# Kernel tuning notes

Measured on AMD Instinct MI355X. Metric: run time of the kernel, lower is better.

Reference implementation:

```python
import jax, jax.numpy as jnp
import numpy as np

H = 16            # num heads
D = 64            # head dim
HID = 1024        # hidden size
ALPHA = 1.0       # < 2 -> power-law kernel
BANDWIDTH = 1.0
A = 0.5           # doubly-stochastic exponent
RADIUS = 1.0      # sphere radius
EPS = 1e-7


def setup_inputs() -> dict:
    key = jax.random.key(0)
    ks = jax.random.split(key, 5)
    x = jax.random.normal(ks[0], (2, 2048, HID), dtype=jnp.float32)
    s = 1.0 / np.sqrt(HID)
    qkv_w = jax.random.normal(ks[1], (3 * HID, HID), dtype=jnp.float32) * s
    qkv_b = jnp.zeros((3 * HID,), dtype=jnp.float32)
    out_w = jax.random.normal(ks[2], (HID, HID), dtype=jnp.float32) * s
    out_b = jnp.zeros((HID,), dtype=jnp.float32)
    return {"x": x, "qkv_w": qkv_w, "qkv_b": qkv_b, "out_w": out_w, "out_b": out_b}


def _l2norm(t):
    # torch F.normalize(p=2, dim=-1): divide by max(||t||, 1e-12)
    n = jnp.sqrt(jnp.sum(t * t, axis=-1, keepdims=True))
    return t / jnp.maximum(n, 1e-12)


def reference(x, qkv_w, qkv_b, out_w, out_b):
    B, S, _ = x.shape
    qkv = x @ qkv_w.T + qkv_b                       # [B,S,3*HID]
    q, k, v = jnp.split(qkv, 3, axis=-1)
    # [B,H,S,D]
    q = _l2norm(q.reshape(B, S, H, D).transpose(0, 2, 1, 3))
    k = _l2norm(k.reshape(B, S, H, D).transpose(0, 2, 1, 3))
    v = v.reshape(B, S, H, D).transpose(0, 2, 1, 3)
    # geodesic distance on the sphere
    cos = jnp.clip(jnp.einsum('bhsd,bhtd->bhst', q, k), -1.0 + EPS, 1.0 - EPS)
    g_dist = jnp.arccos(cos) * RADIUS               # [B,H,S,S]
    # alpha < 2: power-law kernel
    attn_score = (1.0 + g_dist / jnp.sqrt(BANDWIDTH)) ** (-(D + ALPHA))
    # doubly-stochastic-style rescale: diag(row^-a) @ K @ diag(col^-a)
    row = attn_score.sum(-1) ** (-A)                # [B,H,S]
    col = attn_score.sum(-2) ** (-A)                # [B,H,S]
    k_tilde = row[..., :, None] * attn_score * col[..., None, :]
    # F.normalize(p=1, dim=3): divide by max(sum |.|, 1e-12); entries >= 0
    probs = k_tilde / jnp.maximum(k_tilde.sum(-1, keepdims=True), 1e-12)
    out = jnp.einsum('bhst,bhtd->bhsd', probs, v)   # [B,H,S,D]
    out = out.transpose(0, 2, 1, 3).reshape(B, S, HID)
    return out @ out_w.T + out_b
```

## Files before the change

### kernel.cpp

```cpp
#include <hip/hip_runtime.h>
#include <math.h>

#define NH   16
#define HD   64
#define HIDN 1024
#define NB   2
#define SEQ  2048
#define ROWS (NB*SEQ)
#define BH   (NB*NH)

typedef __attribute__((ext_vector_type(8))) short bf16x8;
typedef __attribute__((ext_vector_type(8))) _Float16 f16x8;
typedef __attribute__((ext_vector_type(4))) float f32x4;
typedef __attribute__((ext_vector_type(2))) float f32x2;
typedef _Float16 f16;

typedef const __attribute__((address_space(1))) void GV;
typedef __attribute__((address_space(3))) void LV;
__device__ __forceinline__ void glds16(const void* g, void* l) {
    __builtin_amdgcn_global_load_lds((GV*)g, (LV*)l, 16, 0, 0);
}

__device__ __forceinline__ unsigned short f2bf(float f) {
    unsigned u = __float_as_uint(f);
    u += 0x7FFF + ((u >> 16) & 1);
    return (unsigned short)(u >> 16);
}
__device__ __forceinline__ bf16x8 ldfrag(const unsigned short* p) {
    return *(const bf16x8*)p;
}
__device__ __forceinline__ f16x8 ldfragh(const f16* p) {
    return *(const f16x8*)p;
}
__device__ __forceinline__ f32x4 mfma16(bf16x8 a, bf16x8 b, f32x4 c) {
    return __builtin_amdgcn_mfma_f32_16x16x32_bf16(a, b, c, 0, 0, 0);
}
__device__ __forceinline__ f32x4 mfma16h(f16x8 a, f16x8 b, f32x4 c) {
    return __builtin_amdgcn_mfma_f32_16x16x32_f16(a, b, c, 0, 0, 0);
}

__device__ __forceinline__ f32x2 log2_1pacos_pair(float c0, float c1) {
    f32x2 u = { fmaxf(1.0f - c0, 0.0f), fmaxf(1.0f - c1, 0.0f) };
    f32x2 s = { __builtin_amdgcn_sqrtf(u.x), __builtin_amdgcn_sqrtf(u.y) };
    f32x2 p = u * 2.68532e-3f + 7.89259e-3f;
    p = u * p + 2.6516504e-2f;
    p = u * p + 1.1785113e-1f;
    p = u * p + 1.4142136f;
    f32x2 t = s * p + 1.0f;
    return (f32x2){ __builtin_amdgcn_logf(t.x), __builtin_amdgcn_logf(t.y) };
}
__device__ __forceinline__ unsigned packbf(f32x2 w) {
    return (__float_as_uint(w.x) >> 16) | (__float_as_uint(w.y) & 0xffff0000u);
}

__global__ __launch_bounds__(256)
void conv_f16(const float* __restrict__ src, f16* __restrict__ dst) {
    int i = (blockIdx.x * 256 + threadIdx.x) * 8;
    float4 a = *(const float4*)(src + i);
    float4 b = *(const float4*)(src + i + 4);
    f16x8 o = { (f16)a.x, (f16)a.y, (f16)a.z, (f16)a.w,
                (f16)b.x, (f16)b.y, (f16)b.z, (f16)b.w };
    *(f16x8*)(dst + i) = o;
}

__global__ __launch_bounds__(256)
void gemm_nt_f16(const f16* __restrict__ A, const f16* __restrict__ B,
                 const float* __restrict__ bias, float* __restrict__ C,
                 int M, int N, int K)
{
    __shared__ f16 As[128 * 32];
    __shared__ f16 Bs[128 * 32];
    const int tid = threadIdx.x;
    const int lane = tid & 63, w = tid >> 6;
    const int ln = lane & 15, lq = lane >> 4;
    const int wm = (w >> 1) * 64, wn = (w & 1) * 64;
    const int m0 = blockIdx.x * 128, n0 = blockIdx.y * 128;

    const int grow = lane >> 2;
    const int gcol = (lane & 3) * 8;
    const f16* Ab = A + (size_t)(m0 + w * 32 + grow) * K + gcol;
    const f16* Bb = B + (size_t)(n0 + w * 32 + grow) * K + gcol;
    f16* Asw = As + (w * 32) * 32;
    f16* Bsw = Bs + (w * 32) * 32;

    f32x4 acc[4][4];
    #pragma unroll
    for (int i = 0; i < 4; ++i)
        #pragma unroll
        for (int j = 0; j < 4; ++j) acc[i][j] = (f32x4){0.f, 0.f, 0.f, 0.f};

    for (int kc = 0; kc < K; kc += 32) {
        __syncthreads();
        #pragma unroll
        for (int i = 0; i < 2; ++i) {
            glds16(Ab + (size_t)(i * 16) * K + kc, Asw + (i * 16) * 32);
            glds16(Bb + (size_t)(i * 16) * K + kc, Bsw + (i * 16) * 32);
        }
        __syncthreads();
        f16x8 af[4], bf[4];
        #pragma unroll
        for (int i = 0; i < 4; ++i)
            af[i] = *(const f16x8*)&As[(wm + i * 16 + ln) * 32 + lq * 8];
        #pragma unroll
        for (int j = 0; j < 4; ++j)
            bf[j] = *(const f16x8*)&Bs[(wn + j * 16 + ln) * 32 + lq * 8];
        #pragma unroll
        for (int i = 0; i < 4; ++i)
            #pragma unroll
            for (int j = 0; j < 4; ++j)
                acc[i][j] = mfma16h(af[i], bf[j], acc[i][j]);
    }

    #pragma unroll
    for (int i = 0; i < 4; ++i) {
        #pragma unroll
        for (int j = 0; j < 4; ++j) {
            int colIdx = n0 + wn + j * 16 + ln;
            float bs = bias[colIdx];
            #pragma unroll
            for (int r = 0; r < 4; ++r) {
                int row = m0 + wm + i * 16 + lq * 4 + r;
                C[(size_t)row * N + colIdx] = acc[i][j][r] + bs;
            }
        }
    }
}

__global__ __launch_bounds__(256)
void normalize_qk_f16(const float* __restrict__ qkv,
                      f16* __restrict__ qf, f16* __restrict__ kf)
{
    int w    = blockIdx.x * 4 + (threadIdx.x >> 6);
    int lane = threadIdx.x & 63;
    int n = w >> 4, h = w & 15;
    int b = n >> 11, s = n & 2047;
    const float* base = qkv + (size_t)n * 3 * HIDN + h * HD;
    float q = base[lane], k = base[HIDN + lane];
    float qs = q * q, ks = k * k;
    #pragma unroll
    for (int o = 32; o; o >>= 1) { qs += __shfl_xor(qs, o); ks += __shfl_xor(ks, o); }
    q *= 1.0f / fmaxf(sqrtf(qs), 1e-12f);
    k *= 1.0f / fmaxf(sqrtf(ks), 1e-12f);
    size_t idx = ((size_t)((b * NH + h) * SEQ + s)) * HD + lane;
    qf[idx] = (f16)q;
    kf[idx] = (f16)k;
}

__global__ __launch_bounds__(256)
void v_transpose(const float* __restrict__ qkv, unsigned short* __restrict__ vth)
{
    __shared__ float Ls[64][65];
    int bh = blockIdx.y, s0 = blockIdx.x * 64;
    int b = bh >> 4, h = bh & 15;
    int tid = threadIdx.x;
    #pragma unroll
    for (int i = 0; i < 4; ++i) {
        int idx = tid + i * 256;
        int row = idx >> 4, c4 = (idx & 15) * 4;
        float4 v = *(const float4*)&qkv[((size_t)(b * SEQ + s0 + row)) * 3 * HIDN
                                        + 2 * HIDN + h * HD + c4];
        Ls[row][c4+0] = v.x; Ls[row][c4+1] = v.y; Ls[row][c4+2] = v.z; Ls[row][c4+3] = v.w;
    }
    __syncthreads();
    int d = tid >> 2, sb = (tid & 3) * 16;
    unsigned short hi[16];
    #pragma unroll
    for (int j = 0; j < 16; ++j) hi[j] = f2bf(Ls[sb + j][d]);
    size_t o = ((size_t)bh * HD + d) * SEQ + s0 + sb;
    *(uint4*)&vth[o]     = *(uint4*)&hi[0];
    *(uint4*)&vth[o + 8] = *(uint4*)&hi[8];
}

#define KSTR 72
#define VSTR 40
#define WSTR 40

__global__ __launch_bounds__(256)
void col_sum_f16(const f16* __restrict__ qf, const f16* __restrict__ kf,
                 float* __restrict__ colp)
{
    __shared__ __align__(16) f16 Qs[64 * KSTR];
    int bh = blockIdx.y;
    int tid = threadIdx.x, w = tid >> 6, lane = tid & 63, ln = lane & 15, lq = lane >> 4;
    int m0 = blockIdx.x * 64 + w * 16;
    const int sb0 = blockIdx.z * (SEQ / 128);
    const f16* qb = qf + (size_t)bh * SEQ * HD;
    const int sr = tid >> 3;
    const int sc = (tid & 7) * 8;

    size_t rowK = ((size_t)bh * SEQ + m0 + ln) * HD;
    f16x8 kf0 = ldfragh(kf + rowK + lq * 8), kf1 = ldfragh(kf + rowK + 32 + lq * 8);

    uint4 qa = *(const uint4*)(qb + (size_t)(sb0 * 64 + sr) * HD + sc);
    uint4 qc = *(const uint4*)(qb + (size_t)(sb0 * 64 + sr + 32) * HD + sc);

    f32x2 cacc01 = {0.f, 0.f}, cacc23 = {0.f, 0.f};
    #pragma unroll 1
    for (int st = sb0; st < sb0 + SEQ / 128; ++st) {
        __syncthreads();
        *(uint4*)&Qs[sr * KSTR + sc] = qa;
        *(uint4*)&Qs[(sr + 32) * KSTR + sc] = qc;
        int sn = (st + 1 < sb0 + SEQ / 128) ? (st + 1) * 64 : sb0 * 64;
        qa = *(const uint4*)(qb + (size_t)(sn + sr) * HD + sc);
        qc = *(const uint4*)(qb + (size_t)(sn + sr + 32) * HD + sc);
        __syncthreads();
        #pragma unroll
        for (int nt = 0; nt < 4; ++nt) {
            const f16* qp = &Qs[(nt * 16 + ln) * KSTR + lq * 8];
            f32x4 sacc = {0.f, 0.f, 0.f, 0.f};
            sacc = mfma16h(kf0, *(const f16x8*)qp, sacc);
            sacc = mfma16h(kf1, *(const f16x8*)(qp + 32), sacc);
            f32x2 l01 = log2_1pacos_pair(sacc[0], sacc[1]) * -65.0f;
            f32x2 l23 = log2_1pacos_pair(sacc[2], sacc[3]) * -65.0f;
            cacc01 += (f32x2){ __builtin_amdgcn_exp2f(l01.x),
                               __builtin_amdgcn_exp2f(l01.y) };
            cacc23 += (f32x2){ __builtin_amdgcn_exp2f(l23.x),
                               __builtin_amdgcn_exp2f(l23.y) };
        }
    }
    float cacc[4] = {cacc01.x, cacc01.y, cacc23.x, cacc23.y};
    #pragma unroll
    for (int r = 0; r < 4; ++r) {
        float v = cacc[r];
        v += __shfl_xor(v, 1); v += __shfl_xor(v, 2);
        v += __shfl_xor(v, 4); v += __shfl_xor(v, 8);
        if (ln == 0)
            colp[(size_t)blockIdx.z * BH * SEQ + (size_t)bh * SEQ + m0 + lq * 4 + r] = v;
    }
}

__global__ __launch_bounds__(256)
void col_finalize(const float* __restrict__ colp, float* __restrict__ col)
{
    int i = (blockIdx.x * 256 + threadIdx.x) * 4;
    float4 a = *(const float4*)&colp[i];
    float4 b = *(const float4*)&colp[(size_t)BH * SEQ + i];
    float4 o;
    o.x = -0.5f * __builtin_amdgcn_logf(a.x + b.x);
    o.y = -0.5f * __builtin_amdgcn_logf(a.y + b.y);
    o.z = -0.5f * __builtin_amdgcn_logf(a.z + b.z);
    o.w = -0.5f * __builtin_amdgcn_logf(a.w + b.w);
    *(float4*)&col[i] = o;
}

__global__ __launch_bounds__(256)
void attn_f16(const f16* __restrict__ qf, const f16* __restrict__ kf,
              const unsigned short* __restrict__ vth,
              const float* __restrict__ col,
              float* __restrict__ numb, float* __restrict__ denb)
{
    __shared__ __align__(16) f16 Ks[32 * KSTR];
    __shared__ __align__(16) unsigned short Vs[64 * VSTR];
    __shared__ __align__(16) unsigned short Ws[4][16 * WSTR];
    __shared__ __align__(16) float lcls[32];
    int bh = blockIdx.y;
    int b = bh >> 4, h = bh & 15;
    int tid = threadIdx.x, w = tid >> 6, lane = tid & 63, ln = lane & 15, lq = lane >> 4;
    int m0 = blockIdx.x * 64 + w * 16;
    const int th = blockIdx.z;
    const int tb = th * (SEQ / 2);
    unsigned short* ws = Ws[w];

    const f16* kb = kf + (size_t)bh * SEQ * HD;
    const unsigned short* vb = vth + (size_t)bh * HD * SEQ;
    const float* cb = col + (size_t)bh * SEQ;

    const int krow = tid >> 3;
    const int kcol = (tid & 7) * 8;
    const int vrow = tid >> 2;
    const int vcol = (tid & 3) * 8;

    size_t rowQ = ((size_t)bh * SEQ + m0 + ln) * HD;
    f16x8 qf0 = ldfragh(qf + rowQ + lq * 8), qf1 = ldfragh(qf + rowQ + 32 + lq * 8);

    bf16x8 ones;
    #pragma unroll
    for (int i = 0; i < 8; ++i) ones[i] = (short)0x3F80;

    f32x4 num[4];
    #pragma unroll
    for (int nt = 0; nt < 4; ++nt) num[nt] = (f32x4){0.f, 0.f, 0.f, 0.f};
    f32x4 den = {0.f, 0.f, 0.f, 0.f};

    uint4 ka = *(const uint4*)(kb + (size_t)(tb + krow) * HD + kcol);
    uint4 va = *(const uint4*)(vb + (size_t)vrow * SEQ + tb + vcol);
    float clv = (tid < 32) ? cb[tb + tid] : 0.f;

    #pragma unroll 1
    for (int tt = 0; tt < SEQ / 64; ++tt) {
        __syncthreads();
        *(uint4*)&Ks[krow * KSTR + kcol] = ka;
        *(uint4*)&Vs[vrow * VSTR + vcol] = va;
        if (tid < 32) lcls[tid] = clv;
        int tn = (tt + 1 < SEQ / 64) ? tb + (tt + 1) * 32 : tb;
        ka = *(const uint4*)(kb + (size_t)(tn + krow) * HD + kcol);
        va = *(const uint4*)(vb + (size_t)vrow * SEQ + tn + vcol);
        clv = (tid < 32) ? cb[tn + tid] : 0.f;
        __syncthreads();

        #pragma unroll
        for (int nt = 0; nt < 2; ++nt) {
            const f16* kp = &Ks[(nt * 16 + ln) * KSTR + lq * 8];
            f32x4 sacc = {0.f, 0.f, 0.f, 0.f};
            sacc = mfma16h(*(const f16x8*)kp, qf0, sacc);
            sacc = mfma16h(*(const f16x8*)(kp + 32), qf1, sacc);
            float4 cl = *(const float4*)&lcls[nt * 16 + lq * 4];
            f32x2 a01 = log2_1pacos_pair(sacc[0], sacc[1]) * -65.0f
                        + (f32x2){cl.x, cl.y};
            f32x2 a23 = log2_1pacos_pair(sacc[2], sacc[3]) * -65.0f
                        + (f32x2){cl.z, cl.w};
            f32x2 w01 = { __builtin_amdgcn_exp2f(a01.x),
                          __builtin_amdgcn_exp2f(a01.y) };
            f32x2 w23 = { __builtin_amdgcn_exp2f(a23.x),
                          __builtin_amdgcn_exp2f(a23.y) };
            uint2 pw;
            pw.x = packbf(w01);
            pw.y = packbf(w23);
            *(uint2*)(ws + ln * WSTR + nt * 16 + lq * 4) = pw;
        }
        bf16x8 wa0 = ldfrag(ws + ln * WSTR + lq * 8);
        den = mfma16(wa0, ones, den);
        #pragma unroll
        for (int nt = 0; nt < 4; ++nt) {
            const unsigned short* vp = &Vs[(nt * 16 + ln) * VSTR + lq * 8];
            num[nt] = mfma16(wa0, *(const bf16x8*)vp, num[nt]);
        }
    }

    const size_t noff = (size_t)th * ROWS * HIDN;
    #pragma unroll
    for (int r = 0; r < 4; ++r) {
        int s = m0 + lq * 4 + r;
        #pragma unroll
        for (int nt = 0; nt < 4; ++nt)
            numb[noff + ((size_t)(b * SEQ + s)) * HIDN + h * HD + nt * 16 + ln] =
                num[nt][r];
        if (ln == 0)
            denb[(size_t)th * BH * SEQ + (size_t)bh * SEQ + s] = den[r];
    }
}

__global__ __launch_bounds__(256)
void finalize_ctx(const float* __restrict__ numb, const float* __restrict__ denb,
                  f16* __restrict__ ctx)
{
    size_t i = ((size_t)blockIdx.x * 256 + threadIdx.x) * 8;
    int row = (int)(i >> 10);
    int cidx = (int)(i & (HIDN - 1));
    int b = row >> 11, s = row & 2047;
    int h = cidx >> 6;
    size_t di = (size_t)(b * NH + h) * SEQ + s;
    float d = denb[di] + denb[(size_t)BH * SEQ + di];
    float inv = 1.0f / fmaxf(d, 1e-12f);
    const float* n1 = numb + (size_t)ROWS * HIDN;
    float4 a0 = *(const float4*)&numb[i];
    float4 a1 = *(const float4*)&numb[i + 4];
    float4 b0 = *(const float4*)&n1[i];
    float4 b1 = *(const float4*)&n1[i + 4];
    f16x8 o = { (f16)((a0.x + b0.x) * inv), (f16)((a0.y + b0.y) * inv),
                (f16)((a0.z + b0.z) * inv), (f16)((a0.w + b0.w) * inv),
                (f16)((a1.x + b1.x) * inv), (f16)((a1.y + b1.y) * inv),
                (f16)((a1.z + b1.z) * inv), (f16)((a1.w + b1.w) * inv) };
    *(f16x8*)(ctx + i) = o;
}

extern "C" void kernel_launch(void* const* d_in, const int* in_sizes, int n_in,
                              void* d_out, int out_size, void* d_ws, size_t ws_size,
                              hipStream_t stream) {
    const float* x      = (const float*)d_in[0];
    const float* qkv_w  = (const float*)d_in[1];
    const float* qkv_b  = (const float*)d_in[2];
    const float* out_w  = (const float*)d_in[3];
    const float* out_b  = (const float*)d_in[4];
    float* out = (float*)d_out;

    const size_t NTT = (size_t)BH * SEQ * HD;
    float* qkv = (float*)d_ws;
    float* colp = qkv;
    float* denb = qkv + 2 * (size_t)BH * SEQ;
    float* numb = qkv + 4 * (size_t)BH * SEQ;
    float* col = qkv + (size_t)ROWS * 3 * HIDN;
    f16* xh    = (f16*)(col + (size_t)BH * SEQ);
    f16* wqh   = xh + (size_t)ROWS * HIDN;
    f16* woh   = wqh + (size_t)3 * HIDN * HIDN;
    f16* ctxh  = woh + (size_t)HIDN * HIDN;
    f16* qfp   = ctxh + (size_t)ROWS * HIDN;
    f16* kfp   = qfp + NTT;
    unsigned short* vth = (unsigned short*)(kfp + NTT);

    conv_f16<<<ROWS*HIDN/2048, 256, 0, stream>>>(x, xh);
    conv_f16<<<3*HIDN*HIDN/2048, 256, 0, stream>>>(qkv_w, wqh);
    conv_f16<<<HIDN*HIDN/2048, 256, 0, stream>>>(out_w, woh);

    gemm_nt_f16<<<dim3(ROWS/128, 3*HIDN/128), 256, 0, stream>>>(
        xh, wqh, qkv_b, qkv, ROWS, 3*HIDN, HIDN);
    normalize_qk_f16<<<ROWS*NH/4, 256, 0, stream>>>(qkv, qfp, kfp);
    v_transpose<<<dim3(SEQ/64, BH), 256, 0, stream>>>(qkv, vth);
    col_sum_f16<<<dim3(SEQ/64, BH, 2), 256, 0, stream>>>(qfp, kfp, colp);
    col_finalize<<<BH*SEQ/1024, 256, 0, stream>>>(colp, col);
    attn_f16<<<dim3(SEQ/64, BH, 2), 256, 0, stream>>>(qfp, kfp, vth, col,
                                                      numb, denb);
    finalize_ctx<<<ROWS*HIDN/2048, 256, 0, stream>>>(numb, denb, ctxh);
    gemm_nt_f16<<<dim3(ROWS/128, HIDN/128), 256, 0, stream>>>(
        ctxh, woh, out_b, out, ROWS, HIDN, HIDN);
}
```

Before: 331.4 us.

## Load K/Q/V MFMA fragments directly from global memory, dropping LDS staging and barriers

In the column-sum and attention kernels, the cooperative LDS staging of Q, K, V and column scales, along with the two __syncthreads per tile, is removed. Each wave now reads its MFMA fragments straight from global memory, relying on L1/L2 for reuse across the four waves of a block. The attention tile also grows from 32 to 64 keys per iteration, issuing two bf16 MFMAs per V subtile. This cuts barrier and LDS traffic but leaves more latency exposed on global loads, since the explicit register prefetch of the next tile is gone.

```diff
diff --git a/kernel.cpp b/kernel.cpp
--- a/kernel.cpp
+++ b/kernel.cpp
@@ -171,45 +171,32 @@
     *(uint4*)&vth[o + 8] = *(uint4*)&hi[8];
 }
 
-#define KSTR 72
-#define VSTR 40
-#define WSTR 40
+#define WSTR 72
 
 __global__ __launch_bounds__(256)
 void col_sum_f16(const f16* __restrict__ qf, const f16* __restrict__ kf,
                  float* __restrict__ colp)
 {
-    __shared__ __align__(16) f16 Qs[64 * KSTR];
     int bh = blockIdx.y;
     int tid = threadIdx.x, w = tid >> 6, lane = tid & 63, ln = lane & 15, lq = lane >> 4;
     int m0 = blockIdx.x * 64 + w * 16;
-    const int sb0 = blockIdx.z * (SEQ / 128);
+    const int sb0 = blockIdx.z * (SEQ / 2);
     const f16* qb = qf + (size_t)bh * SEQ * HD;
-    const int sr = tid >> 3;
-    const int sc = (tid & 7) * 8;
 
     size_t rowK = ((size_t)bh * SEQ + m0 + ln) * HD;
     f16x8 kf0 = ldfragh(kf + rowK + lq * 8), kf1 = ldfragh(kf + rowK + 32 + lq * 8);
 
-    uint4 qa = *(const uint4*)(qb + (size_t)(sb0 * 64 + sr) * HD + sc);
-    uint4 qc = *(const uint4*)(qb + (size_t)(sb0 * 64 + sr + 32) * HD + sc);
-
     f32x2 cacc01 = {0.f, 0.f}, cacc23 = {0.f, 0.f};
     #pragma unroll 1
-    for (int st = sb0; st < sb0 + SEQ / 128; ++st) {
-        __syncthreads();
-        *(uint4*)&Qs[sr * KSTR + sc] = qa;
-        *(uint4*)&Qs[(sr + 32) * KSTR + sc] = qc;
-        int sn = (st + 1 < sb0 + SEQ / 128) ? (st + 1) * 64 : sb0 * 64;
-        qa = *(const uint4*)(qb + (size_t)(sn + sr) * HD + sc);
-        qc = *(const uint4*)(qb + (size_t)(sn + sr + 32) * HD + sc);
-        __syncthreads();
+    for (int st = 0; st < SEQ / 128; ++st) {
+        int s0 = sb0 + st * 64;
         #pragma unroll
         for (int nt = 0; nt < 4; ++nt) {
-            const f16* qp = &Qs[(nt * 16 + ln) * KSTR + lq * 8];
+            const f16* qp = qb + (size_t)(s0 + nt * 16 + ln) * HD + lq * 8;
+            f16x8 qa = ldfragh(qp), qc = ldfragh(qp + 32);
             f32x4 sacc = {0.f, 0.f, 0.f, 0.f};
-            sacc = mfma16h(kf0, *(const f16x8*)qp, sacc);
-            sacc = mfma16h(kf1, *(const f16x8*)(qp + 32), sacc);
+            sacc = mfma16h(kf0, qa, sacc);
+            sacc = mfma16h(kf1, qc, sacc);
             f32x2 l01 = log2_1pacos_pair(sacc[0], sacc[1]) * -65.0f;
             f32x2 l23 = log2_1pacos_pair(sacc[2], sacc[3]) * -65.0f;
             cacc01 += (f32x2){ __builtin_amdgcn_exp2f(l01.x),
@@ -249,10 +236,7 @@
               const float* __restrict__ col,
               float* __restrict__ numb, float* __restrict__ denb)
 {
-    __shared__ __align__(16) f16 Ks[32 * KSTR];
-    __shared__ __align__(16) unsigned short Vs[64 * VSTR];
     __shared__ __align__(16) unsigned short Ws[4][16 * WSTR];
-    __shared__ __align__(16) float lcls[32];
     int bh = blockIdx.y;
     int b = bh >> 4, h = bh & 15;
     int tid = threadIdx.x, w = tid >> 6, lane = tid & 63, ln = lane & 15, lq = lane >> 4;
@@ -265,11 +249,6 @@
     const unsigned short* vb = vth + (size_t)bh * HD * SEQ;
     const float* cb = col + (size_t)bh * SEQ;
 
-    const int krow = tid >> 3;
-    const int kcol = (tid & 7) * 8;
-    const int vrow = tid >> 2;
-    const int vcol = (tid & 3) * 8;
-
     size_t rowQ = ((size_t)bh * SEQ + m0 + ln) * HD;
     f16x8 qf0 = ldfragh(qf + rowQ + lq * 8), qf1 = ldfragh(qf + rowQ + 32 + lq * 8);
 
@@ -282,29 +261,17 @@
     for (int nt = 0; nt < 4; ++nt) num[nt] = (f32x4){0.f, 0.f, 0.f, 0.f};
     f32x4 den = {0.f, 0.f, 0.f, 0.f};
 
-    uint4 ka = *(const uint4*)(kb + (size_t)(tb + krow) * HD + kcol);
-    uint4 va = *(const uint4*)(vb + (size_t)vrow * SEQ + tb + vcol);
-    float clv = (tid < 32) ? cb[tb + tid] : 0.f;
-
     #pragma unroll 1
-    for (int tt = 0; tt < SEQ / 64; ++tt) {
-        __syncthreads();
-        *(uint4*)&Ks[krow * KSTR + kcol] = ka;
-        *(uint4*)&Vs[vrow * VSTR + vcol] = va;
-        if (tid < 32) lcls[tid] = clv;
-        int tn = (tt + 1 < SEQ / 64) ? tb + (tt + 1) * 32 : tb;
-        ka = *(const uint4*)(kb + (size_t)(tn + krow) * HD + kcol);
-        va = *(const uint4*)(vb + (size_t)vrow * SEQ + tn + vcol);
-        clv = (tid < 32) ? cb[tn + tid] : 0.f;
-        __syncthreads();
-
-        #pragma unroll
-        for (int nt = 0; nt < 2; ++nt) {
-            const f16* kp = &Ks[(nt * 16 + ln) * KSTR + lq * 8];
+    for (int tt = 0; tt < SEQ / 128; ++tt) {
+        int t0 = tb + tt * 64;
+        #pragma unroll
+        for (int nt = 0; nt < 4; ++nt) {
+            const f16* kp = kb + (size_t)(t0 + nt * 16 + ln) * HD + lq * 8;
+            f16x8 ka = ldfragh(kp), kc = ldfragh(kp + 32);
             f32x4 sacc = {0.f, 0.f, 0.f, 0.f};
-            sacc = mfma16h(*(const f16x8*)kp, qf0, sacc);
-            sacc = mfma16h(*(const f16x8*)(kp + 32), qf1, sacc);
-            float4 cl = *(const float4*)&lcls[nt * 16 + lq * 4];
+            sacc = mfma16h(ka, qf0, sacc);
+            sacc = mfma16h(kc, qf1, sacc);
+            float4 cl = *(const float4*)&cb[t0 + nt * 16 + lq * 4];
             f32x2 a01 = log2_1pacos_pair(sacc[0], sacc[1]) * -65.0f
                         + (f32x2){cl.x, cl.y};
             f32x2 a23 = log2_1pacos_pair(sacc[2], sacc[3]) * -65.0f
@@ -319,11 +286,14 @@
             *(uint2*)(ws + ln * WSTR + nt * 16 + lq * 4) = pw;
         }
         bf16x8 wa0 = ldfrag(ws + ln * WSTR + lq * 8);
+        bf16x8 wa1 = ldfrag(ws + ln * WSTR + 32 + lq * 8);
         den = mfma16(wa0, ones, den);
+        den = mfma16(wa1, ones, den);
         #pragma unroll
         for (int nt = 0; nt < 4; ++nt) {
-            const unsigned short* vp = &Vs[(nt * 16 + ln) * VSTR + lq * 8];
+            const unsigned short* vp = vb + (size_t)(nt * 16 + ln) * SEQ + t0 + lq * 8;
             num[nt] = mfma16(wa0, *(const bf16x8*)vp, num[nt]);
+            num[nt] = mfma16(wa1, *(const bf16x8*)(vp + 32), num[nt]);
         }
     }
 
```

Result: slower. 537.1 us (+62.1%).
